# Kernel optimization log

Measured on AMD Instinct MI355X. Metric: run time of the kernel, lower is better.

The kernel has to match this reference:

```python
import jax, jax.numpy as jnp
import numpy as np

B, S, H = 2, 2048, 2048
NH, D_CKV, D_CQ, DR, DHV = 16, 512, 768, 64, 128
DH = H // NH            # 128 per-head content dim
SCALE = (DR + DH) ** -0.5


def apply_rope(x, freq):
    # x: [b, nh, s, d], freq: [s, d//2] angles; rotate interleaved pairs
    cos = jnp.cos(freq)
    sin = jnp.sin(freq)
    x1 = x[..., 0::2]
    x2 = x[..., 1::2]
    o1 = x1 * cos - x2 * sin
    o2 = x1 * sin + x2 * cos
    return jnp.stack([o1, o2], axis=-1).reshape(x.shape)


def setup_inputs() -> dict:
    key = jax.random.key(0)
    ks = jax.random.split(key, 16)
    w = lambda k, shape: jax.random.normal(k, shape, jnp.float32) * 0.02
    x = jax.random.normal(ks[0], (B, S, H), jnp.float32)
    # rotary angles: pos * inv_freq, shape [S, DR//2]
    inv = 1.0 / (10000.0 ** (jnp.arange(0, DR, 2, dtype=jnp.float32) / DR))
    freq = jnp.arange(S, dtype=jnp.float32)[:, None] * inv[None, :]
    mask = jnp.tril(jnp.ones((S, S), dtype=bool))[None, None]  # causal
    return {
        'x': x, 'freq': freq, 'mask': mask,
        'w_dq': w(ks[1], (H, D_CQ)),          'b_dq': jnp.zeros((D_CQ,), jnp.float32),
        'w_uq': w(ks[2], (D_CQ, NH * DH)),    'b_uq': jnp.zeros((NH * DH,), jnp.float32),
        'w_qr': w(ks[3], (D_CQ, NH * DR)),    'b_qr': jnp.zeros((NH * DR,), jnp.float32),
        'w_dkv': w(ks[4], (H, D_CKV)),        'b_dkv': jnp.zeros((D_CKV,), jnp.float32),
        'w_ukv': w(ks[5], (D_CKV, NH * (DH + DHV))), 'b_ukv': jnp.zeros((NH * (DH + DHV),), jnp.float32),
        'w_kr': w(ks[6], (H, DR)),            'b_kr': jnp.zeros((DR,), jnp.float32),
        'w_o': w(ks[7], (NH * DHV, H)),       'b_o': jnp.zeros((H,), jnp.float32),
    }


def reference(x, freq, mask, w_dq, b_dq, w_uq, b_uq, w_qr, b_qr,
              w_dkv, b_dkv, w_ukv, b_ukv, w_kr, b_kr, w_o, b_o):
    b, s, _ = x.shape
    # query branch: low-rank compression then up-projection
    c_q = x @ w_dq + b_dq                                   # [b,s,d_cq]
    q_c = (c_q @ w_uq + b_uq).reshape(b, s, NH, DH).transpose(0, 2, 1, 3)
    q_r = (c_q @ w_qr + b_qr).reshape(b, s, NH, DR).transpose(0, 2, 1, 3)
    q_r = apply_rope(q_r, freq)
    q = jnp.concatenate([q_c, q_r], axis=-1)               # [b,nh,s,dh+dr]
    # key/value branch: shared kv latent + shared rope key
    c_kv = x @ w_dkv + b_dkv                                # [b,s,d_ckv]
    kv_c = (c_kv @ w_ukv + b_ukv).reshape(b, s, NH, DH + DHV)
    k_c = kv_c[..., :DH].transpose(0, 2, 1, 3)              # [b,nh,s,dh]
    v_c = kv_c[..., DH:].transpose(0, 2, 1, 3)              # [b,nh,s,dhv]
    k_r = (x @ w_kr + b_kr).reshape(b, s, 1, DR).transpose(0, 2, 1, 3)
    k_r = apply_rope(k_r, freq)
    k_r = jnp.broadcast_to(k_r, (b, NH, s, DR))
    k = jnp.concatenate([k_c, k_r], axis=-1)               # [b,nh,s,dh+dr]
    # manual attention
    scores = jnp.einsum('bhsd,bhtd->bhst', q, k) * SCALE
    scores = jnp.where(mask, scores, -jnp.inf)
    attn = jax.nn.softmax(scores, axis=-1)
    out = jnp.einsum('bhst,bhtv->bhsv', attn, v_c)
    out = out.transpose(0, 2, 1, 3).reshape(b, s, NH * DHV)
    return out @ w_o + b_o
```

## Files before the change

### kernel.cpp

```cpp
#include <hip/hip_runtime.h>
#include <cstdint>
#include <cstddef>

#define S_LEN 2048
#define SCALE_L2E (0.07216878364870323f * 1.4426950408889634f)

typedef __attribute__((ext_vector_type(8))) short short8;
typedef __attribute__((ext_vector_type(4))) float f32x4;
typedef __attribute__((ext_vector_type(16))) float f32x16;
typedef __attribute__((ext_vector_type(4))) unsigned short ushort4v;

__device__ __forceinline__ unsigned short f2bf(float f) {
  unsigned int u = __builtin_bit_cast(unsigned int, f);
  u += 0x7FFFu + ((u >> 16) & 1u);
  return (unsigned short)(u >> 16);
}
__device__ __forceinline__ float bf2f(unsigned short h) {
  unsigned int u = ((unsigned int)h) << 16;
  return __builtin_bit_cast(float, u);
}
__device__ __forceinline__ unsigned int cvt_pk_bf16(float lo, float hi) {
  unsigned int r;
  asm("v_cvt_pk_bf16_f32 %0, %1, %2" : "=v"(r) : "v"(lo), "v"(hi));
  return r;
}
__device__ __forceinline__ float exp2_raw(float x) {
  return __builtin_amdgcn_exp2f(x);
}

typedef const __attribute__((address_space(1))) void* gas_ptr;
typedef __attribute__((address_space(3))) void* las_ptr;
__device__ __forceinline__ void gload16(const void* g, void* l) {
  __builtin_amdgcn_global_load_lds((gas_ptr)g, (las_ptr)l, 16, 0, 0);
}


__device__ __forceinline__ void transpose_tile(
    const float* __restrict__ src, unsigned short* __restrict__ dst,
    int K, int N, int kb, int nb, unsigned short* tile) {
  const int tid = threadIdx.x;
  #pragma unroll
  for (int i = 0; i < 4; ++i) {
    int idx = i * 256 + tid;
    int row = idx >> 4, c4 = (idx & 15) << 2;
    const float4 v = *reinterpret_cast<const float4*>(&src[(size_t)(kb + row) * N + nb + c4]);
    tile[row * 72 + c4 + 0] = f2bf(v.x);
    tile[row * 72 + c4 + 1] = f2bf(v.y);
    tile[row * 72 + c4 + 2] = f2bf(v.z);
    tile[row * 72 + c4 + 3] = f2bf(v.w);
  }
  __syncthreads();
  #pragma unroll
  for (int i = 0; i < 4; ++i) {
    int idx = i * 256 + tid;
    int n = idx >> 4, kc = (idx & 15) << 2;
    ushort4v o = { tile[(kc + 0) * 72 + n], tile[(kc + 1) * 72 + n],
                   tile[(kc + 2) * 72 + n], tile[(kc + 3) * 72 + n] };
    *reinterpret_cast<ushort4v*>(&dst[(size_t)(nb + n) * K + kb + kc]) = o;
  }
}

template <int MODE>
__device__ __forceinline__ void gemm_body(
    const unsigned short* __restrict__ A, const unsigned short* __restrict__ Bt,
    const float* __restrict__ bias, void* __restrict__ Cout,
    unsigned short* __restrict__ Vt, int N, int K, int lda, int ldc,
    int subId, int subN, int gx, unsigned short* SM) {
  unsigned short* As = SM;
  unsigned short* Bs = SM + 8192;
  const int tid = threadIdx.x;
  const int lane = tid & 63, wid = tid >> 6;
  const int wr = wid >> 1, wc = wid & 1;
  const int l = (subId & 7) * (subN >> 3) + (subId >> 3);
  const int m0 = (l / gx) << 7, n0 = (l % gx) << 7;
  const int l15 = lane & 15, g = lane >> 4;

  const int srow = (wid << 5) + (lane >> 2);
  const int scol = (lane & 3) << 3;
  const unsigned short* aptr0 = &A[(size_t)(m0 + srow) * lda + scol];
  const unsigned short* aptr1 = &A[(size_t)(m0 + srow + 16) * lda + scol];
  int br0 = n0 + srow;      if (br0 >= N) br0 = N - 1;
  int br1 = n0 + srow + 16; if (br1 >= N) br1 = N - 1;
  const unsigned short* bptr0 = &Bt[(size_t)br0 * K + scol];
  const unsigned short* bptr1 = &Bt[(size_t)br1 * K + scol];
  const int lofs0 = ((wid << 1) + 0) << 9;
  const int lofs1 = ((wid << 1) + 1) << 9;

  f32x4 acc[4][4];
  #pragma unroll
  for (int m = 0; m < 4; ++m)
    #pragma unroll
    for (int n = 0; n < 4; ++n) acc[m][n] = f32x4{0.f, 0.f, 0.f, 0.f};

  gload16(aptr0, &As[lofs0]);
  gload16(aptr1, &As[lofs1]);
  gload16(bptr0, &Bs[lofs0]);
  gload16(bptr1, &Bs[lofs1]);
  __syncthreads();

  int cur = 0;
  for (int k0 = 0; k0 < K; k0 += 32) {
    const int nxt = cur ^ 1;
    if (k0 + 32 < K) {
      gload16(aptr0 + k0 + 32, &As[nxt * 4096 + lofs0]);
      gload16(aptr1 + k0 + 32, &As[nxt * 4096 + lofs1]);
      gload16(bptr0 + k0 + 32, &Bs[nxt * 4096 + lofs0]);
      gload16(bptr1 + k0 + 32, &Bs[nxt * 4096 + lofs1]);
    }
    short8 af[4], bfr[4];
    #pragma unroll
    for (int m = 0; m < 4; ++m)
      af[m] = *reinterpret_cast<const short8*>(
          &As[cur * 4096 + (((wr << 6) + (m << 4) + l15) << 5) + (g << 3)]);
    #pragma unroll
    for (int n = 0; n < 4; ++n)
      bfr[n] = *reinterpret_cast<const short8*>(
          &Bs[cur * 4096 + (((wc << 6) + (n << 4) + l15) << 5) + (g << 3)]);
    __builtin_amdgcn_s_setprio(1);
    #pragma unroll
    for (int m = 0; m < 4; ++m)
      #pragma unroll
      for (int n = 0; n < 4; ++n)
        acc[m][n] = __builtin_amdgcn_mfma_f32_16x16x32_bf16(af[m], bfr[n], acc[m][n], 0, 0, 0);
    __builtin_amdgcn_s_setprio(0);
    __syncthreads();
    cur = nxt;
  }

  if (MODE == 2 && (n0 & 128)) {
    const int hh = n0 >> 8;
    const int bb = m0 >> 11;
    const int s0 = m0 & 2047;
    unsigned short* T = SM;
    #pragma unroll
    for (int pass = 0; pass < 2; ++pass) {
      __syncthreads();
      if (wc == pass) {
        #pragma unroll
        for (int n = 0; n < 4; ++n) {
          int c = (n << 4) + l15;
          float bv = bias[n0 + (pass << 6) + c];
          #pragma unroll
          for (int m = 0; m < 4; ++m) {
            int rb = (wr << 6) + (m << 4) + (g << 2);
            #pragma unroll
            for (int r = 0; r < 4; ++r)
              T[c * 130 + rb + r] = f2bf(acc[m][n][r] + bv);
          }
        }
      }
      __syncthreads();
      int c = tid >> 2, seg = tid & 3;
      const unsigned short* src = &T[c * 130 + (seg << 5)];
      unsigned int wbuf[16];
      #pragma unroll
      for (int i = 0; i < 16; ++i)
        wbuf[i] = *reinterpret_cast<const unsigned int*>(&src[i * 2]);
      int4* dst = reinterpret_cast<int4*>(
          &Vt[(((size_t)bb * 16 + hh) * 128 + (pass << 6) + c) * 2048 + s0 + (seg << 5)]);
      #pragma unroll
      for (int i = 0; i < 4; ++i) {
        int4 v;
        v.x = (int)wbuf[4 * i + 0]; v.y = (int)wbuf[4 * i + 1];
        v.z = (int)wbuf[4 * i + 2]; v.w = (int)wbuf[4 * i + 3];
        dst[i] = v;
      }
    }
    return;
  }

  #pragma unroll
  for (int n = 0; n < 4; ++n) {
    int col = n0 + (wc << 6) + (n << 4) + l15;
    if (col >= N) continue;
    float bv = bias[col];
    #pragma unroll
    for (int m = 0; m < 4; ++m) {
      int rowb = m0 + (wr << 6) + (m << 4) + (g << 2);
      #pragma unroll
      for (int r = 0; r < 4; ++r) {
        float v = acc[m][n][r] + bv;
        int row = rowb + r;
        if (MODE == 0) {
          reinterpret_cast<float*>(Cout)[(size_t)row * ldc + col] = v;
        } else if (MODE == 1) {
          reinterpret_cast<unsigned short*>(Cout)[(size_t)row * ldc + col] = f2bf(v);
        } else {
          int hh = col >> 8, dd = col & 255;
          reinterpret_cast<unsigned short*>(Cout)[(size_t)row * 2048 + hh * 128 + dd] = f2bf(v);
        }
      }
    }
  }
}


__global__ __launch_bounds__(256) void k_prep_a(
    const float* __restrict__ x, const float* __restrict__ freq,
    const float* __restrict__ wdq, const float* __restrict__ wdkv,
    const float* __restrict__ wkr,
    const float* __restrict__ b_uq, const float* __restrict__ b_qr,
    const float* __restrict__ b_dq, const float* __restrict__ b_dkv,
    const float* __restrict__ b_kr,
    unsigned short* __restrict__ x_bf, unsigned short* __restrict__ wd_t,
    float* __restrict__ tab, float* __restrict__ bcat, float* __restrict__ ball) {
  __shared__ __align__(16) unsigned short SMEM[64 * 72];
  const int bid = blockIdx.x;
  const int tid = threadIdx.x;
  if (bid < 384) {
    transpose_tile(wdq, wd_t, 2048, 768, (bid / 12) << 6, (bid % 12) << 6, SMEM);
  } else if (bid < 640) {
    int r = bid - 384;
    transpose_tile(wdkv, wd_t + (size_t)768 * 2048, 2048, 512, (r >> 3) << 6, (r & 7) << 6, SMEM);
  } else if (bid < 672) {
    int r = bid - 640;
    transpose_tile(wkr, wd_t + (size_t)1280 * 2048, 2048, 64, r << 6, 0, SMEM);
  } else if (bid < 8864) {
    int i = (bid - 672) * 256 + tid;
    const float4 v = reinterpret_cast<const float4*>(x)[i];
    ushort4v o = { f2bf(v.x), f2bf(v.y), f2bf(v.z), f2bf(v.w) };
    reinterpret_cast<ushort4v*>(x_bf)[i] = o;
  } else if (bid < 9120) {
    int i = (bid - 8864) * 256 + tid;
    float f = freq[i];
    tab[2 * i] = cosf(f);
    tab[2 * i + 1] = sinf(f);
  } else {
    int i = (bid - 9120) * 256 + tid;
    if (i < 2048) bcat[i] = b_uq[i];
    else if (i < 3072) bcat[i] = b_qr[i - 2048];
    else if (i < 3840) ball[i - 3072] = b_dq[i - 3072];
    else if (i < 4352) ball[i - 3072] = b_dkv[i - 3840];
    else if (i < 4416) ball[i - 3072] = b_kr[i - 4352];
  }
}

__global__ __launch_bounds__(256) void k_down(
    const unsigned short* __restrict__ x_bf, const unsigned short* __restrict__ wd_t,
    const float* __restrict__ ball, unsigned short* __restrict__ c_all,
    const float* __restrict__ wuq, const float* __restrict__ wqr,
    const float* __restrict__ wukv, const float* __restrict__ wo,
    unsigned short* __restrict__ wqc_t, unsigned short* __restrict__ wukv_t,
    unsigned short* __restrict__ wo_t) {
  __shared__ __align__(16) unsigned short SMEM[16384];
  const int bid = blockIdx.x;
  if (bid < 352) {
    gemm_body<1>(x_bf, wd_t, ball, c_all, nullptr, 1344, 2048, 2048, 1344,
                 bid, 352, 11, SMEM);
  } else if (bid < 736) {
    int r = bid - 352;
    transpose_tile(wuq, wqc_t, 768, 2048, (r >> 5) << 6, (r & 31) << 6, SMEM);
  } else if (bid < 928) {
    int r = bid - 736;
    transpose_tile(wqr, wqc_t + (size_t)2048 * 768, 768, 1024, (r >> 4) << 6, (r & 15) << 6, SMEM);
  } else if (bid < 1440) {
    int r = bid - 928;
    transpose_tile(wukv, wukv_t, 512, 4096, (r >> 6) << 6, (r & 63) << 6, SMEM);
  } else {
    int r = bid - 1440;
    transpose_tile(wo, wo_t, 2048, 2048, (r >> 5) << 6, (r & 31) << 6, SMEM);
  }
}

__global__ __launch_bounds__(256) void k_up(
    const unsigned short* __restrict__ c_all, const unsigned short* __restrict__ wqc_t,
    const float* __restrict__ bcat, unsigned short* __restrict__ q_raw,
    const unsigned short* __restrict__ wukv_t, const float* __restrict__ b_ukv,
    unsigned short* __restrict__ kc, unsigned short* __restrict__ v_t,
    const float* __restrict__ tab, unsigned short* __restrict__ krro) {
  __shared__ __align__(16) unsigned short SMEM[16384];
  const int bid = blockIdx.x;
  if (bid < 768) {
    gemm_body<1>(c_all, wqc_t, bcat, q_raw, nullptr, 3072, 768, 1344, 3072,
                 bid, 768, 24, SMEM);
  } else if (bid < 1792) {
    gemm_body<2>(c_all + 768, wukv_t, b_ukv, kc, v_t, 4096, 512, 1344, 2048,
                 bid - 768, 1024, 32, SMEM);
  } else {
    int idx = (bid - 1792) * 256 + threadIdx.x;
    if (idx < 4096 * 32) {
      int bs = idx >> 5, p = idx & 31;
      int s = bs & (S_LEN - 1);
      float c = tab[(s * 32 + p) * 2], sn = tab[(s * 32 + p) * 2 + 1];
      float x1 = bf2f(c_all[(size_t)bs * 1344 + 1280 + 2 * p]);
      float x2 = bf2f(c_all[(size_t)bs * 1344 + 1280 + 2 * p + 1]);
      krro[bs * 64 + 2 * p] = f2bf(x1 * c - x2 * sn);
      krro[bs * 64 + 2 * p + 1] = f2bf(x1 * sn + x2 * c);
    }
  }
}

__global__ __launch_bounds__(256) void k_out(
    const unsigned short* __restrict__ attn, const unsigned short* __restrict__ wo_t,
    const float* __restrict__ b_o, float* __restrict__ out) {
  __shared__ __align__(16) unsigned short SMEM[16384];
  gemm_body<0>(attn, wo_t, b_o, out, nullptr, 2048, 2048, 2048, 2048,
               (int)blockIdx.x, 512, 16, SMEM);
}

__global__ __launch_bounds__(512, 2) void k_mla_attn(
    const unsigned short* __restrict__ q_raw, const unsigned short* __restrict__ kc,
    const unsigned short* __restrict__ v_t, const unsigned short* __restrict__ krro,
    const float* __restrict__ tab, unsigned short* __restrict__ attn_out) {
  __shared__ __align__(16) unsigned char smem[110592];
  unsigned short* KcB = reinterpret_cast<unsigned short*>(smem);
  unsigned short* VtB = reinterpret_cast<unsigned short*>(smem + 49152);
  float* Msh = reinterpret_cast<float*>(smem);

  const int tid = threadIdx.x;
  const int lane = tid & 63, w = tid >> 6;
  const int s = w & 3, e = w >> 2;
  const int l31 = lane & 31, hi = lane >> 5;
  const int hi8 = hi << 3;
  const int bid = blockIdx.x;
  const int bh = bid & 31, b = bh >> 4, h = bh & 15;
  const int uu = (bid >> 5) & 7;
  const int chunk = (bid >> 8) ? (15 - uu) : uu;
  const size_t bsb = (size_t)b * S_LEN;

  const int krow0 = (s << 3) + (lane >> 4);
  const int kunit = lane & 15;
  const int vd = (w << 4) + (lane >> 2);
  const int vu = lane & 3;
  const size_t vrow = ((size_t)(b * 16 + h) * 128 + vd) * 2048;

  const int q0 = (chunk << 7) + (s << 5);
  const int srow = q0 + l31;
  const int ntb = (chunk << 2) + 4;
  const int U = ntb >> 1;
  const int nt_w = (q0 + 63) >> 5;

  short8 qf[12];
  {
    const size_t qrow = (bsb + q0 + l31) * 3072;
    #pragma unroll
    for (int ks = 0; ks < 8; ++ks) {
      short8 rv = *reinterpret_cast<const short8*>(&q_raw[qrow + h * 128 + ks * 16 + hi8]);
      union { unsigned short us[8]; short8 v; } uq;
      #pragma unroll
      for (int j = 0; j < 8; ++j)
        uq.us[j] = f2bf(bf2f((unsigned short)rv[j]) * SCALE_L2E);
      qf[ks] = uq.v;
    }
    #pragma unroll
    for (int f = 0; f < 4; ++f) {
      short8 rv = *reinterpret_cast<const short8*>(
          &q_raw[qrow + 2048 + h * 64 + f * 16 + hi8]);
      int pi0 = 8 * f + 4 * hi;
      union { unsigned short us[8]; short8 v; } uq;
      #pragma unroll
      for (int j = 0; j < 4; ++j) {
        float c = tab[(srow * 32 + pi0 + j) * 2];
        float sn = tab[(srow * 32 + pi0 + j) * 2 + 1];
        float x1 = bf2f((unsigned short)rv[2 * j]);
        float x2 = bf2f((unsigned short)rv[2 * j + 1]);
        uq.us[2 * j] = f2bf((x1 * c - x2 * sn) * SCALE_L2E);
        uq.us[2 * j + 1] = f2bf((x1 * sn + x2 * c) * SCALE_L2E);
      }
      qf[8 + f] = uq.v;
    }
  }

  f32x16 acc[4];
  #pragma unroll
  for (int a = 0; a < 4; ++a)
    #pragma unroll
    for (int r = 0; r < 16; ++r) acc[a][r] = 0.f;
  float mrun = -1e30f, lsum = 0.f;

  short8 krf_cur[4], krf_nxt[4];
  int4 vcA, vcB;
  {
    #pragma unroll
    for (int f = 0; f < 4; ++f)
      krf_cur[f] = *reinterpret_cast<const short8*>(
          &krro[(bsb + e * 32 + l31) * 64 + f * 16 + hi8]);
    #pragma unroll
    for (int i = 0; i < 2; ++i) {
      const int ts = e + 2 * i;
      gload16(&kc[(bsb + (ts << 5) + krow0) * 2048 + h * 128 + (kunit ^ (krow0 & 15)) * 8],
              &KcB[(ts % 6) * 4096 + (krow0 << 7)]);
      gload16(&kc[(bsb + (ts << 5) + krow0 + 4) * 2048 + h * 128 + (kunit ^ ((krow0 + 4) & 15)) * 8],
              &KcB[(ts % 6) * 4096 + ((krow0 + 4) << 7)]);
    }
    #pragma unroll
    for (int tv = 0; tv < 4; ++tv) {
      int4 vv = *reinterpret_cast<const int4*>(&v_t[vrow + (tv << 5) + (vu << 3)]);
      *reinterpret_cast<int4*>(&VtB[tv * 5120 + vd * 40 + (vu << 3)]) = vv;
    }
    vcA = *reinterpret_cast<const int4*>(&v_t[vrow + (4 << 5) + (vu << 3)]);
    vcB = *reinterpret_cast<const int4*>(&v_t[vrow + (5 << 5) + (vu << 3)]);
  }
  __syncthreads();

  for (int u = 0; u < U; ++u) {
    const int t = (u << 1) + e;
    int tvA = (u << 1) + 6; int sA = tvA > 63 ? 63 : tvA;
    int tvB = tvA + 1;      int sB = tvB > 63 ? 63 : tvB;
    int4 vnA = *reinterpret_cast<const int4*>(&v_t[vrow + (sA << 5) + (vu << 3)]);
    int4 vnB = *reinterpret_cast<const int4*>(&v_t[vrow + (sB << 5) + (vu << 3)]);
    {
      int t2 = t + 2; if (t2 > 63) t2 = 63;
      #pragma unroll
      for (int f = 0; f < 4; ++f)
        krf_nxt[f] = *reinterpret_cast<const short8*>(
            &krro[(bsb + (t2 << 5) + l31) * 64 + f * 16 + hi8]);
    }
    {
      int tsK = (u << 1) + 4 + e;
      int src = tsK > 63 ? 63 : tsK;
      int kb = tsK % 6;
      gload16(&kc[(bsb + (src << 5) + krow0) * 2048 + h * 128 + (kunit ^ (krow0 & 15)) * 8],
              &KcB[kb * 4096 + (krow0 << 7)]);
      gload16(&kc[(bsb + (src << 5) + krow0 + 4) * 2048 + h * 128 + (kunit ^ ((krow0 + 4) & 15)) * 8],
              &KcB[kb * 4096 + ((krow0 + 4) << 7)]);
    }

    if (t < nt_w) {
      const int kvb = t << 5;
      const int kbuf = t % 6;

      f32x16 sca, scb;
      #pragma unroll
      for (int r = 0; r < 16; ++r) { sca[r] = 0.f; scb[r] = 0.f; }
      __builtin_amdgcn_s_setprio(1);
      #pragma unroll
      for (int j = 0; j < 4; ++j) {
        short8 k0 = *reinterpret_cast<const short8*>(
            &KcB[kbuf * 4096 + (l31 << 7) + ((((2 * (2 * j)) | hi) ^ (l31 & 15)) << 3)]);
        sca = __builtin_amdgcn_mfma_f32_32x32x16_bf16(k0, qf[2 * j], sca, 0, 0, 0);
        short8 k1 = *reinterpret_cast<const short8*>(
            &KcB[kbuf * 4096 + (l31 << 7) + ((((2 * (2 * j + 1)) | hi) ^ (l31 & 15)) << 3)]);
        scb = __builtin_amdgcn_mfma_f32_32x32x16_bf16(k1, qf[2 * j + 1], scb, 0, 0, 0);
      }
      sca = __builtin_amdgcn_mfma_f32_32x32x16_bf16(krf_cur[0], qf[8], sca, 0, 0, 0);
      scb = __builtin_amdgcn_mfma_f32_32x32x16_bf16(krf_cur[1], qf[9], scb, 0, 0, 0);
      sca = __builtin_amdgcn_mfma_f32_32x32x16_bf16(krf_cur[2], qf[10], sca, 0, 0, 0);
      scb = __builtin_amdgcn_mfma_f32_32x32x16_bf16(krf_cur[3], qf[11], scb, 0, 0, 0);
      __builtin_amdgcn_s_setprio(0);
      f32x16 sc = sca + scb;

      if (kvb + 31 > q0) {
        #pragma unroll
        for (int r = 0; r < 16; ++r) {
          int kv = kvb + (r & 3) + ((r >> 2) << 3) + (hi << 2);
          if (kv > srow) sc[r] = -1e30f;
        }
      }
      float m0 = fmaxf(fmaxf(sc[0], sc[1]), fmaxf(sc[2], sc[3]));
      float m1 = fmaxf(fmaxf(sc[4], sc[5]), fmaxf(sc[6], sc[7]));
      float m2 = fmaxf(fmaxf(sc[8], sc[9]), fmaxf(sc[10], sc[11]));
      float m3 = fmaxf(fmaxf(sc[12], sc[13]), fmaxf(sc[14], sc[15]));
      float tmax = fmaxf(fmaxf(m0, m1), fmaxf(m2, m3));
      tmax = fmaxf(tmax, __shfl_xor(tmax, 32));

      bool rescale = !__all(tmax <= mrun + 8.f);
      float scold = 1.f;
      if (rescale) {
        float mm = fmaxf(mrun, tmax);
        scold = exp2_raw(mrun - mm);
        mrun = mm;
      }
      float pe[16];
      float ts = 0.f;
      #pragma unroll
      for (int r = 0; r < 16; ++r) { pe[r] = exp2_raw(sc[r] - mrun); ts += pe[r]; }
      ts += __shfl_xor(ts, 32);
      lsum = lsum * scold + ts;

      if (rescale) {
        #pragma unroll
        for (int a = 0; a < 4; ++a)
          #pragma unroll
          for (int r = 0; r < 16; ++r) acc[a][r] *= scold;
      }
      #pragma unroll
      for (int ks = 0; ks < 2; ++ks) {
        unsigned int X0 = cvt_pk_bf16(pe[8 * ks + 0], pe[8 * ks + 1]);
        unsigned int X1 = cvt_pk_bf16(pe[8 * ks + 2], pe[8 * ks + 3]);
        unsigned int Y0 = cvt_pk_bf16(pe[8 * ks + 4], pe[8 * ks + 5]);
        unsigned int Y1 = cvt_pk_bf16(pe[8 * ks + 6], pe[8 * ks + 7]);
        unsigned int send0 = hi ? X0 : Y0;
        unsigned int send1 = hi ? X1 : Y1;
        unsigned int recv0 = (unsigned int)__shfl_xor((int)send0, 32);
        unsigned int recv1 = (unsigned int)__shfl_xor((int)send1, 32);
        union { unsigned int u[4]; short8 v; } pa;
        pa.u[0] = hi ? recv0 : X0;
        pa.u[1] = hi ? recv1 : X1;
        pa.u[2] = hi ? Y0 : recv0;
        pa.u[3] = hi ? Y1 : recv1;
        __builtin_amdgcn_s_setprio(1);
        #pragma unroll
        for (int a = 0; a < 4; ++a) {
          short8 va = *reinterpret_cast<const short8*>(
              &VtB[kbuf * 5120 + ((a << 5) + l31) * 40 + (((ks << 1) | hi) << 3)]);
          acc[a] = __builtin_amdgcn_mfma_f32_32x32x16_bf16(va, pa.v, acc[a], 0, 0, 0);
        }
        __builtin_amdgcn_s_setprio(0);
      }
    }

    *reinterpret_cast<int4*>(
        &VtB[(((u << 1) + 4) % 6) * 5120 + vd * 40 + (vu << 3)]) = vcA;
    *reinterpret_cast<int4*>(
        &VtB[(((u << 1) + 5) % 6) * 5120 + vd * 40 + (vu << 3)]) = vcB;
    vcA = vnA; vcB = vnB;
    #pragma unroll
    for (int f = 0; f < 4; ++f) krf_cur[f] = krf_nxt[f];
    asm volatile("s_waitcnt vmcnt(8) lgkmcnt(0)" ::: "memory");
    __builtin_amdgcn_s_barrier();
  }

  __syncthreads();

  if (e == 1) {
    #pragma unroll
    for (int a = 0; a < 4; ++a)
      #pragma unroll
      for (int r = 0; r < 16; ++r) {
        int v = 32 * a + (r & 3) + ((r >> 2) << 3) + (hi << 2);
        Msh[((s << 7) + v) * 33 + l31] = acc[a][r];
      }
    if (hi == 0) {
      Msh[16896 + ((s << 5) + l31) * 2 + 0] = mrun;
      Msh[16896 + ((s << 5) + l31) * 2 + 1] = lsum;
    }
  }
  __syncthreads();
  if (e == 0) {
    float m1 = Msh[16896 + ((s << 5) + l31) * 2 + 0];
    float l1 = Msh[16896 + ((s << 5) + l31) * 2 + 1];
    float mm = fmaxf(mrun, m1);
    float ea = exp2_raw(mrun - mm), eb = exp2_raw(m1 - mm);
    float linv = 1.f / (lsum * ea + l1 * eb);
    float al = ea * linv, be = eb * linv;
    #pragma unroll
    for (int a = 0; a < 4; ++a)
      #pragma unroll
      for (int r = 0; r < 16; ++r) {
        int v = 32 * a + (r & 3) + ((r >> 2) << 3) + (hi << 2);
        float part = Msh[((s << 7) + v) * 33 + l31];
        acc[a][r] = acc[a][r] * al + part * be;
      }
    unsigned int* Tb = reinterpret_cast<unsigned int*>(smem) + s * 4224;
    #pragma unroll
    for (int a = 0; a < 4; ++a)
      #pragma unroll
      for (int j = 0; j < 8; ++j) {
        unsigned int word = cvt_pk_bf16(acc[a][2 * j], acc[a][2 * j + 1]);
        int wc = 16 * a + 2 * hi + (j & 1) + 4 * (j >> 1);
        Tb[l31 * 68 + wc] = word;
      }
    const unsigned char* Tbb = reinterpret_cast<const unsigned char*>(Tb);
    #pragma unroll
    for (int u2 = 0; u2 < 8; ++u2) {
      int qr = (u2 << 2) + (lane >> 4);
      int4 rd = *reinterpret_cast<const int4*>(&Tbb[qr * 272 + (lane & 15) * 16]);
      *reinterpret_cast<int4*>(
          &attn_out[(bsb + q0 + qr) * 2048 + h * 128 + (lane & 15) * 8]) = rd;
    }
  }
}


extern "C" void kernel_launch(void* const* d_in, const int* in_sizes, int n_in,
                              void* d_out, int out_size, void* d_ws, size_t ws_size,
                              hipStream_t stream) {
  (void)in_sizes; (void)n_in; (void)out_size; (void)ws_size;
  const float* x = (const float*)d_in[0];
  const float* freq = (const float*)d_in[1];
  const float* w_dq = (const float*)d_in[3];
  const float* b_dq = (const float*)d_in[4];
  const float* w_uq = (const float*)d_in[5];
  const float* b_uq = (const float*)d_in[6];
  const float* w_qr = (const float*)d_in[7];
  const float* b_qr = (const float*)d_in[8];
  const float* w_dkv = (const float*)d_in[9];
  const float* b_dkv = (const float*)d_in[10];
  const float* w_ukv = (const float*)d_in[11];
  const float* b_ukv = (const float*)d_in[12];
  const float* w_kr = (const float*)d_in[13];
  const float* b_kr = (const float*)d_in[14];
  const float* w_o = (const float*)d_in[15];
  const float* b_o = (const float*)d_in[16];

  char* ws = (char*)d_ws;
  size_t off = 0;
  auto alloc = [&](size_t bytes) {
    char* p = ws + off;
    off += (bytes + 255) & ~(size_t)255;
    return p;
  };
  unsigned short* x_bf   = (unsigned short*)alloc((size_t)4096 * 2048 * 2);
  unsigned short* wd_t   = (unsigned short*)alloc((size_t)1344 * 2048 * 2);
  unsigned short* wqc_t  = (unsigned short*)alloc((size_t)3072 * 768 * 2);
  unsigned short* wukv_t = (unsigned short*)alloc((size_t)4096 * 512 * 2);
  unsigned short* wo_t   = (unsigned short*)alloc((size_t)2048 * 2048 * 2);
  float* tab             = (float*)alloc((size_t)2048 * 32 * 2 * 4);
  float* bcat            = (float*)alloc((size_t)3072 * 4);
  float* ball            = (float*)alloc((size_t)1344 * 4);
  unsigned short* c_all  = (unsigned short*)alloc((size_t)4096 * 1344 * 2);
  unsigned short* krro   = (unsigned short*)alloc((size_t)4096 * 64 * 2);
  unsigned short* q_raw  = (unsigned short*)alloc((size_t)4096 * 3072 * 2);
  unsigned short* kc     = (unsigned short*)alloc((size_t)4096 * 2048 * 2);
  unsigned short* v_t    = (unsigned short*)alloc((size_t)4096 * 2048 * 2);
  unsigned short* attn   = (unsigned short*)alloc((size_t)4096 * 2048 * 2);

  k_prep_a<<<dim3(9138), dim3(256), 0, stream>>>(
      x, freq, w_dq, w_dkv, w_kr, b_uq, b_qr, b_dq, b_dkv, b_kr,
      x_bf, wd_t, tab, bcat, ball);

  k_down<<<dim3(2464), dim3(256), 0, stream>>>(
      x_bf, wd_t, ball, c_all, w_uq, w_qr, w_ukv, w_o, wqc_t, wukv_t, wo_t);

  k_up<<<dim3(2304), dim3(256), 0, stream>>>(
      c_all, wqc_t, bcat, q_raw, wukv_t, b_ukv, kc, v_t, tab, krro);

  k_mla_attn<<<dim3(512), dim3(512), 0, stream>>>(q_raw, kc, v_t, krro, tab, attn);

  k_out<<<dim3(512), dim3(256), 0, stream>>>(attn, wo_t, b_o, (float*)d_out);
}
```

Measured before the change: 250.0 us.

## Restructure MLA attention pipeline to process two KV tiles per warp per barrier

The attention loop now advances four KV tiles per iteration (two per warp group) instead of two, which halves the number of block barriers. The direct global-to-LDS K loads are replaced by register-staged loads into an 8-slot ring, and the XOR swizzle is dropped in favour of a padded row stride. Rope-key fragments are loaded just before use instead of being prefetched. The aim is to cut synchronisation overhead and deepen prefetching. The cost is more LDS (which may reduce occupancy below the two-block launch bound), more registers, and krro loads that now sit on the critical path.

Measured after the change: 246.8 us (median of 3 runs). No clear change (-1.3%).

```diff
diff --git a/kernel.cpp b/kernel.cpp
--- a/kernel.cpp
+++ b/kernel.cpp
@@ -302,9 +302,9 @@
     const unsigned short* __restrict__ q_raw, const unsigned short* __restrict__ kc,
     const unsigned short* __restrict__ v_t, const unsigned short* __restrict__ krro,
     const float* __restrict__ tab, unsigned short* __restrict__ attn_out) {
-  __shared__ __align__(16) unsigned char smem[110592];
+  __shared__ __align__(16) unsigned char smem[151552];
   unsigned short* KcB = reinterpret_cast<unsigned short*>(smem);
-  unsigned short* VtB = reinterpret_cast<unsigned short*>(smem + 49152);
+  unsigned short* VtB = reinterpret_cast<unsigned short*>(smem + 69632);
   float* Msh = reinterpret_cast<float*>(smem);
 
   const int tid = threadIdx.x;
@@ -320,14 +320,14 @@
 
   const int krow0 = (s << 3) + (lane >> 4);
   const int kunit = lane & 15;
+  const unsigned short* kcbase = &kc[bsb * 2048 + h * 128 + kunit * 8];
   const int vd = (w << 4) + (lane >> 2);
   const int vu = lane & 3;
-  const size_t vrow = ((size_t)(b * 16 + h) * 128 + vd) * 2048;
+  const unsigned short* vtbase = &v_t[((size_t)(b * 16 + h) * 128 + vd) * 2048 + vu * 8];
 
   const int q0 = (chunk << 7) + (s << 5);
   const int srow = q0 + l31;
-  const int ntb = (chunk << 2) + 4;
-  const int U = ntb >> 1;
+  const int U = chunk + 1;
   const int nt_w = (q0 + 63) >> 5;
 
   short8 qf[12];
@@ -368,146 +368,171 @@
     for (int r = 0; r < 16; ++r) acc[a][r] = 0.f;
   float mrun = -1e30f, lsum = 0.f;
 
-  short8 krf_cur[4], krf_nxt[4];
-  int4 vcA, vcB;
+  auto process_tile = [&](int t, const short8* krf) {
+    const int kvb = t << 5;
+    const int kbuf = t & 7;
+    f32x16 sca, scb;
+    #pragma unroll
+    for (int r = 0; r < 16; ++r) { sca[r] = 0.f; scb[r] = 0.f; }
+    __builtin_amdgcn_s_setprio(1);
+    #pragma unroll
+    for (int j = 0; j < 4; ++j) {
+      short8 k0 = *reinterpret_cast<const short8*>(
+          &KcB[kbuf * 4352 + l31 * 136 + (((j << 2) | hi) << 3)]);
+      sca = __builtin_amdgcn_mfma_f32_32x32x16_bf16(k0, qf[2 * j], sca, 0, 0, 0);
+      short8 k1 = *reinterpret_cast<const short8*>(
+          &KcB[kbuf * 4352 + l31 * 136 + ((((j << 2) + 2) | hi) << 3)]);
+      scb = __builtin_amdgcn_mfma_f32_32x32x16_bf16(k1, qf[2 * j + 1], scb, 0, 0, 0);
+    }
+    sca = __builtin_amdgcn_mfma_f32_32x32x16_bf16(krf[0], qf[8], sca, 0, 0, 0);
+    scb = __builtin_amdgcn_mfma_f32_32x32x16_bf16(krf[1], qf[9], scb, 0, 0, 0);
+    sca = __builtin_amdgcn_mfma_f32_32x32x16_bf16(krf[2], qf[10], sca, 0, 0, 0);
+    scb = __builtin_amdgcn_mfma_f32_32x32x16_bf16(krf[3], qf[11], scb, 0, 0, 0);
+    __builtin_amdgcn_s_setprio(0);
+    f32x16 sc = sca + scb;
+
+    if (kvb + 31 > q0) {
+      #pragma unroll
+      for (int r = 0; r < 16; ++r) {
+        int kv = kvb + (r & 3) + ((r >> 2) << 3) + (hi << 2);
+        if (kv > srow) sc[r] = -1e30f;
+      }
+    }
+    float m0 = fmaxf(fmaxf(sc[0], sc[1]), fmaxf(sc[2], sc[3]));
+    float m1 = fmaxf(fmaxf(sc[4], sc[5]), fmaxf(sc[6], sc[7]));
+    float m2 = fmaxf(fmaxf(sc[8], sc[9]), fmaxf(sc[10], sc[11]));
+    float m3 = fmaxf(fmaxf(sc[12], sc[13]), fmaxf(sc[14], sc[15]));
+    float tmax = fmaxf(fmaxf(m0, m1), fmaxf(m2, m3));
+    tmax = fmaxf(tmax, __shfl_xor(tmax, 32));
+
+    bool rescale = !__all(tmax <= mrun + 8.f);
+    float scold = 1.f;
+    if (rescale) {
+      float mm = fmaxf(mrun, tmax);
+      scold = exp2_raw(mrun - mm);
+      mrun = mm;
+    }
+    float pe[16];
+    float ts = 0.f;
+    #pragma unroll
+    for (int r = 0; r < 16; ++r) { pe[r] = exp2_raw(sc[r] - mrun); ts += pe[r]; }
+    ts += __shfl_xor(ts, 32);
+    lsum = lsum * scold + ts;
+
+    if (rescale) {
+      #pragma unroll
+      for (int a = 0; a < 4; ++a)
+        #pragma unroll
+        for (int r = 0; r < 16; ++r) acc[a][r] *= scold;
+    }
+    #pragma unroll
+    for (int ks = 0; ks < 2; ++ks) {
+      unsigned int X0 = cvt_pk_bf16(pe[8 * ks + 0], pe[8 * ks + 1]);
+      unsigned int X1 = cvt_pk_bf16(pe[8 * ks + 2], pe[8 * ks + 3]);
+      unsigned int Y0 = cvt_pk_bf16(pe[8 * ks + 4], pe[8 * ks + 5]);
+      unsigned int Y1 = cvt_pk_bf16(pe[8 * ks + 6], pe[8 * ks + 7]);
+      unsigned int send0 = hi ? X0 : Y0;
+      unsigned int send1 = hi ? X1 : Y1;
+      unsigned int recv0 = (unsigned int)__shfl_xor((int)send0, 32);
+      unsigned int recv1 = (unsigned int)__shfl_xor((int)send1, 32);
+      union { unsigned int u[4]; short8 v; } pa;
+      pa.u[0] = hi ? recv0 : X0;
+      pa.u[1] = hi ? recv1 : X1;
+      pa.u[2] = hi ? Y0 : recv0;
+      pa.u[3] = hi ? Y1 : recv1;
+      __builtin_amdgcn_s_setprio(1);
+      #pragma unroll
+      for (int a = 0; a < 4; ++a) {
+        short8 va = *reinterpret_cast<const short8*>(
+            &VtB[kbuf * 5120 + ((a << 5) + l31) * 40 + (((ks << 1) | hi) << 3)]);
+        acc[a] = __builtin_amdgcn_mfma_f32_32x32x16_bf16(va, pa.v, acc[a], 0, 0, 0);
+      }
+      __builtin_amdgcn_s_setprio(0);
+    }
+  };
+
+  int4 kcur0a, kcur0b, kcur1a, kcur1b;
+  int4 vcur0, vcur1, vcur2, vcur3;
   {
-    #pragma unroll
-    for (int f = 0; f < 4; ++f)
-      krf_cur[f] = *reinterpret_cast<const short8*>(
-          &krro[(bsb + e * 32 + l31) * 64 + f * 16 + hi8]);
-    #pragma unroll
-    for (int i = 0; i < 2; ++i) {
-      const int ts = e + 2 * i;
-      gload16(&kc[(bsb + (ts << 5) + krow0) * 2048 + h * 128 + (kunit ^ (krow0 & 15)) * 8],
-              &KcB[(ts % 6) * 4096 + (krow0 << 7)]);
-      gload16(&kc[(bsb + (ts << 5) + krow0 + 4) * 2048 + h * 128 + (kunit ^ ((krow0 + 4) & 15)) * 8],
-              &KcB[(ts % 6) * 4096 + ((krow0 + 4) << 7)]);
-    }
-    #pragma unroll
-    for (int tv = 0; tv < 4; ++tv) {
-      int4 vv = *reinterpret_cast<const int4*>(&v_t[vrow + (tv << 5) + (vu << 3)]);
-      *reinterpret_cast<int4*>(&VtB[tv * 5120 + vd * 40 + (vu << 3)]) = vv;
-    }
-    vcA = *reinterpret_cast<const int4*>(&v_t[vrow + (4 << 5) + (vu << 3)]);
-    vcB = *reinterpret_cast<const int4*>(&v_t[vrow + (5 << 5) + (vu << 3)]);
+    const int t0 = 2 * e, t1 = 2 * e + 1;
+    int4 a0 = *reinterpret_cast<const int4*>(&kcbase[(size_t)((t0 << 5) + krow0) * 2048]);
+    int4 a1 = *reinterpret_cast<const int4*>(&kcbase[(size_t)((t0 << 5) + krow0 + 4) * 2048]);
+    int4 b0 = *reinterpret_cast<const int4*>(&kcbase[(size_t)((t1 << 5) + krow0) * 2048]);
+    int4 b1 = *reinterpret_cast<const int4*>(&kcbase[(size_t)((t1 << 5) + krow0 + 4) * 2048]);
+    int4 v0 = *reinterpret_cast<const int4*>(&vtbase[0 << 5]);
+    int4 v1 = *reinterpret_cast<const int4*>(&vtbase[1 << 5]);
+    int4 v2 = *reinterpret_cast<const int4*>(&vtbase[2 << 5]);
+    int4 v3 = *reinterpret_cast<const int4*>(&vtbase[3 << 5]);
+    *reinterpret_cast<int4*>(&KcB[(t0 & 7) * 4352 + krow0 * 136 + kunit * 8]) = a0;
+    *reinterpret_cast<int4*>(&KcB[(t0 & 7) * 4352 + (krow0 + 4) * 136 + kunit * 8]) = a1;
+    *reinterpret_cast<int4*>(&KcB[(t1 & 7) * 4352 + krow0 * 136 + kunit * 8]) = b0;
+    *reinterpret_cast<int4*>(&KcB[(t1 & 7) * 4352 + (krow0 + 4) * 136 + kunit * 8]) = b1;
+    *reinterpret_cast<int4*>(&VtB[0 * 5120 + vd * 40 + vu * 8]) = v0;
+    *reinterpret_cast<int4*>(&VtB[1 * 5120 + vd * 40 + vu * 8]) = v1;
+    *reinterpret_cast<int4*>(&VtB[2 * 5120 + vd * 40 + vu * 8]) = v2;
+    *reinterpret_cast<int4*>(&VtB[3 * 5120 + vd * 40 + vu * 8]) = v3;
+    const int n0t = 4 + 2 * e, n1t = 5 + 2 * e;
+    kcur0a = *reinterpret_cast<const int4*>(&kcbase[(size_t)((n0t << 5) + krow0) * 2048]);
+    kcur0b = *reinterpret_cast<const int4*>(&kcbase[(size_t)((n0t << 5) + krow0 + 4) * 2048]);
+    kcur1a = *reinterpret_cast<const int4*>(&kcbase[(size_t)((n1t << 5) + krow0) * 2048]);
+    kcur1b = *reinterpret_cast<const int4*>(&kcbase[(size_t)((n1t << 5) + krow0 + 4) * 2048]);
+    vcur0 = *reinterpret_cast<const int4*>(&vtbase[4 << 5]);
+    vcur1 = *reinterpret_cast<const int4*>(&vtbase[5 << 5]);
+    vcur2 = *reinterpret_cast<const int4*>(&vtbase[6 << 5]);
+    vcur3 = *reinterpret_cast<const int4*>(&vtbase[7 << 5]);
   }
   __syncthreads();
 
   for (int u = 0; u < U; ++u) {
-    const int t = (u << 1) + e;
-    int tvA = (u << 1) + 6; int sA = tvA > 63 ? 63 : tvA;
-    int tvB = tvA + 1;      int sB = tvB > 63 ? 63 : tvB;
-    int4 vnA = *reinterpret_cast<const int4*>(&v_t[vrow + (sA << 5) + (vu << 3)]);
-    int4 vnB = *reinterpret_cast<const int4*>(&v_t[vrow + (sB << 5) + (vu << 3)]);
     {
-      int t2 = t + 2; if (t2 > 63) t2 = 63;
-      #pragma unroll
-      for (int f = 0; f < 4; ++f)
-        krf_nxt[f] = *reinterpret_cast<const short8*>(
-            &krro[(bsb + (t2 << 5) + l31) * 64 + f * 16 + hi8]);
+      const int wk0 = (4 * u + 4 + 2 * e) & 7, wk1 = (4 * u + 5 + 2 * e) & 7;
+      *reinterpret_cast<int4*>(&KcB[wk0 * 4352 + krow0 * 136 + kunit * 8]) = kcur0a;
+      *reinterpret_cast<int4*>(&KcB[wk0 * 4352 + (krow0 + 4) * 136 + kunit * 8]) = kcur0b;
+      *reinterpret_cast<int4*>(&KcB[wk1 * 4352 + krow0 * 136 + kunit * 8]) = kcur1a;
+      *reinterpret_cast<int4*>(&KcB[wk1 * 4352 + (krow0 + 4) * 136 + kunit * 8]) = kcur1b;
+      const int wv = (4 * u + 4) & 7;
+      *reinterpret_cast<int4*>(&VtB[wv * 5120 + vd * 40 + vu * 8]) = vcur0;
+      *reinterpret_cast<int4*>(&VtB[((wv + 1) & 7) * 5120 + vd * 40 + vu * 8]) = vcur1;
+      *reinterpret_cast<int4*>(&VtB[((wv + 2) & 7) * 5120 + vd * 40 + vu * 8]) = vcur2;
+      *reinterpret_cast<int4*>(&VtB[((wv + 3) & 7) * 5120 + vd * 40 + vu * 8]) = vcur3;
     }
     {
-      int tsK = (u << 1) + 4 + e;
-      int src = tsK > 63 ? 63 : tsK;
-      int kb = tsK % 6;
-      gload16(&kc[(bsb + (src << 5) + krow0) * 2048 + h * 128 + (kunit ^ (krow0 & 15)) * 8],
-              &KcB[kb * 4096 + (krow0 << 7)]);
-      gload16(&kc[(bsb + (src << 5) + krow0 + 4) * 2048 + h * 128 + (kunit ^ ((krow0 + 4) & 15)) * 8],
-              &KcB[kb * 4096 + ((krow0 + 4) << 7)]);
-    }
-
-    if (t < nt_w) {
-      const int kvb = t << 5;
-      const int kbuf = t % 6;
-
-      f32x16 sca, scb;
-      #pragma unroll
-      for (int r = 0; r < 16; ++r) { sca[r] = 0.f; scb[r] = 0.f; }
-      __builtin_amdgcn_s_setprio(1);
-      #pragma unroll
-      for (int j = 0; j < 4; ++j) {
-        short8 k0 = *reinterpret_cast<const short8*>(
-            &KcB[kbuf * 4096 + (l31 << 7) + ((((2 * (2 * j)) | hi) ^ (l31 & 15)) << 3)]);
-        sca = __builtin_amdgcn_mfma_f32_32x32x16_bf16(k0, qf[2 * j], sca, 0, 0, 0);
-        short8 k1 = *reinterpret_cast<const short8*>(
-            &KcB[kbuf * 4096 + (l31 << 7) + ((((2 * (2 * j + 1)) | hi) ^ (l31 & 15)) << 3)]);
-        scb = __builtin_amdgcn_mfma_f32_32x32x16_bf16(k1, qf[2 * j + 1], scb, 0, 0, 0);
-      }
-      sca = __builtin_amdgcn_mfma_f32_32x32x16_bf16(krf_cur[0], qf[8], sca, 0, 0, 0);
-      scb = __builtin_amdgcn_mfma_f32_32x32x16_bf16(krf_cur[1], qf[9], scb, 0, 0, 0);
-      sca = __builtin_amdgcn_mfma_f32_32x32x16_bf16(krf_cur[2], qf[10], sca, 0, 0, 0);
-      scb = __builtin_amdgcn_mfma_f32_32x32x16_bf16(krf_cur[3], qf[11], scb, 0, 0, 0);
-      __builtin_amdgcn_s_setprio(0);
-      f32x16 sc = sca + scb;
-
-      if (kvb + 31 > q0) {
+      int t0 = 4 * u + 8 + 2 * e; if (t0 > 63) t0 = 63;
+      int t1 = 4 * u + 9 + 2 * e; if (t1 > 63) t1 = 63;
+      kcur0a = *reinterpret_cast<const int4*>(&kcbase[(size_t)((t0 << 5) + krow0) * 2048]);
+      kcur0b = *reinterpret_cast<const int4*>(&kcbase[(size_t)((t0 << 5) + krow0 + 4) * 2048]);
+      kcur1a = *reinterpret_cast<const int4*>(&kcbase[(size_t)((t1 << 5) + krow0) * 2048]);
+      kcur1b = *reinterpret_cast<const int4*>(&kcbase[(size_t)((t1 << 5) + krow0 + 4) * 2048]);
+      int tv0 = 4 * u + 8;  if (tv0 > 63) tv0 = 63;
+      int tv1 = 4 * u + 9;  if (tv1 > 63) tv1 = 63;
+      int tv2 = 4 * u + 10; if (tv2 > 63) tv2 = 63;
+      int tv3 = 4 * u + 11; if (tv3 > 63) tv3 = 63;
+      vcur0 = *reinterpret_cast<const int4*>(&vtbase[tv0 << 5]);
+      vcur1 = *reinterpret_cast<const int4*>(&vtbase[tv1 << 5]);
+      vcur2 = *reinterpret_cast<const int4*>(&vtbase[tv2 << 5]);
+      vcur3 = *reinterpret_cast<const int4*>(&vtbase[tv3 << 5]);
+    }
+    {
+      const int tA = 4 * u + 2 * e;
+      if (tA < nt_w) {
+        short8 krfA[4];
         #pragma unroll
-        for (int r = 0; r < 16; ++r) {
-          int kv = kvb + (r & 3) + ((r >> 2) << 3) + (hi << 2);
-          if (kv > srow) sc[r] = -1e30f;
-        }
-      }
-      float m0 = fmaxf(fmaxf(sc[0], sc[1]), fmaxf(sc[2], sc[3]));
-      float m1 = fmaxf(fmaxf(sc[4], sc[5]), fmaxf(sc[6], sc[7]));
-      float m2 = fmaxf(fmaxf(sc[8], sc[9]), fmaxf(sc[10], sc[11]));
-      float m3 = fmaxf(fmaxf(sc[12], sc[13]), fmaxf(sc[14], sc[15]));
-      float tmax = fmaxf(fmaxf(m0, m1), fmaxf(m2, m3));
-      tmax = fmaxf(tmax, __shfl_xor(tmax, 32));
-
-      bool rescale = !__all(tmax <= mrun + 8.f);
-      float scold = 1.f;
-      if (rescale) {
-        float mm = fmaxf(mrun, tmax);
-        scold = exp2_raw(mrun - mm);
-        mrun = mm;
-      }
-      float pe[16];
-      float ts = 0.f;
-      #pragma unroll
-      for (int r = 0; r < 16; ++r) { pe[r] = exp2_raw(sc[r] - mrun); ts += pe[r]; }
-      ts += __shfl_xor(ts, 32);
-      lsum = lsum * scold + ts;
-
-      if (rescale) {
+        for (int f = 0; f < 4; ++f)
+          krfA[f] = *reinterpret_cast<const short8*>(
+              &krro[(bsb + (tA << 5) + l31) * 64 + f * 16 + hi8]);
+        process_tile(tA, krfA);
+      }
+      const int tB = tA + 1;
+      if (tB < nt_w) {
+        short8 krfB[4];
         #pragma unroll
-        for (int a = 0; a < 4; ++a)
-          #pragma unroll
-          for (int r = 0; r < 16; ++r) acc[a][r] *= scold;
-      }
-      #pragma unroll
-      for (int ks = 0; ks < 2; ++ks) {
-        unsigned int X0 = cvt_pk_bf16(pe[8 * ks + 0], pe[8 * ks + 1]);
-        unsigned int X1 = cvt_pk_bf16(pe[8 * ks + 2], pe[8 * ks + 3]);
-        unsigned int Y0 = cvt_pk_bf16(pe[8 * ks + 4], pe[8 * ks + 5]);
-        unsigned int Y1 = cvt_pk_bf16(pe[8 * ks + 6], pe[8 * ks + 7]);
-        unsigned int send0 = hi ? X0 : Y0;
-        unsigned int send1 = hi ? X1 : Y1;
-        unsigned int recv0 = (unsigned int)__shfl_xor((int)send0, 32);
-        unsigned int recv1 = (unsigned int)__shfl_xor((int)send1, 32);
-        union { unsigned int u[4]; short8 v; } pa;
-        pa.u[0] = hi ? recv0 : X0;
-        pa.u[1] = hi ? recv1 : X1;
-        pa.u[2] = hi ? Y0 : recv0;
-        pa.u[3] = hi ? Y1 : recv1;
-        __builtin_amdgcn_s_setprio(1);
-        #pragma unroll
-        for (int a = 0; a < 4; ++a) {
-          short8 va = *reinterpret_cast<const short8*>(
-              &VtB[kbuf * 5120 + ((a << 5) + l31) * 40 + (((ks << 1) | hi) << 3)]);
-          acc[a] = __builtin_amdgcn_mfma_f32_32x32x16_bf16(va, pa.v, acc[a], 0, 0, 0);
-        }
-        __builtin_amdgcn_s_setprio(0);
-      }
-    }
-
-    *reinterpret_cast<int4*>(
-        &VtB[(((u << 1) + 4) % 6) * 5120 + vd * 40 + (vu << 3)]) = vcA;
-    *reinterpret_cast<int4*>(
-        &VtB[(((u << 1) + 5) % 6) * 5120 + vd * 40 + (vu << 3)]) = vcB;
-    vcA = vnA; vcB = vnB;
-    #pragma unroll
-    for (int f = 0; f < 4; ++f) krf_cur[f] = krf_nxt[f];
-    asm volatile("s_waitcnt vmcnt(8) lgkmcnt(0)" ::: "memory");
+        for (int f = 0; f < 4; ++f)
+          krfB[f] = *reinterpret_cast<const short8*>(
+              &krro[(bsb + (tB << 5) + l31) * 64 + f * 16 + hi8]);
+        process_tile(tB, krfB);
+      }
+    }
+    asm volatile("s_waitcnt lgkmcnt(0)" ::: "memory");
     __builtin_amdgcn_s_barrier();
   }
 
```
